# Kernel optimization log

Hardware: AMD Instinct MI355X
Metric: run time of the kernel (lower is better)

The kernel has to match this reference:

```python
import jax, jax.numpy as jnp
import numpy as np

IMG = 224                      # hardcoded image_size in apply_mask
K = int(0.25 * IMG * IMG)      # 12544 pixels masked per sample


def setup_inputs() -> dict:
    key = jax.random.key(0)
    k1, k2 = jax.random.split(key)
    B = 256
    data = jax.random.normal(k1, (B, IMG, IMG, 3), dtype=jnp.float32)
    # |gradients| flattened over (H, W, C) -> length IMG*IMG*3, nonnegative
    line_grad = jax.random.uniform(k2, (B, IMG * IMG * 3), dtype=jnp.float32)
    return {"data": data, "line_grad": line_grad}


def _mask_one(d, g):
    # d: [IMG, IMG, 3], g: [IMG*IMG*3]
    _, idx = jax.lax.top_k(g, K)              # flat indices into (H,W,C)
    reduced = jnp.mod(idx, IMG * IMG)         # fold channel offset -> spatial
    rows = reduced // IMG
    cols = reduced % IMG
    # scatter zeros across all 3 channels at the selected pixels
    return d.at[rows, cols].set(0.0)


def reference(data, line_grad):
    # vectorized_map over the batch -> vmap
    return jax.vmap(_mask_one)(data, line_grad)
```

## Files before the change

kernel.cpp:

```cpp
#include <hip/hip_runtime.h>

#define IMG    224
#define NPIX   (IMG * IMG)
#define NELEM  (NPIX * 3)
#define KSEL   12544
#define NBINS  4096
#define MAXCAND 2048
#define NMASKW (NPIX / 32)
#define NVEC   (NELEM / 4)
#define BLOCK  1024
#define NWAVE  (BLOCK / 64)

typedef float f4 __attribute__((ext_vector_type(4)));

__global__ __launch_bounds__(BLOCK) void masked_model_kernel(
    const float* __restrict__ data,
    const float* __restrict__ grad,
    float* __restrict__ out)
{
    const int b    = blockIdx.x;
    const int tid  = threadIdx.x;
    const int lane = tid & 63;
    const int wid  = tid >> 6;

    const float* g = grad + (size_t)b * NELEM;
    const float* d = data + (size_t)b * NELEM;
    float*       o = out  + (size_t)b * NELEM;

    __shared__ unsigned int hist[NBINS];
    __shared__ unsigned int mask[NMASKW];
    __shared__ unsigned int candkey[MAXCAND];
    __shared__ unsigned int candidx[MAXCAND];
    __shared__ unsigned int wtot[NWAVE];
    __shared__ unsigned int candcnt;
    __shared__ int sB1;
    __shared__ unsigned int sR;

    for (int i = tid; i < NBINS; i += BLOCK) hist[i] = 0u;
    for (int i = tid; i < NMASKW; i += BLOCK) mask[i] = 0u;
    if (tid == 0) candcnt = 0u;
    __syncthreads();

    const f4* g4 = (const f4*)g;

    {
        int i = tid;
        for (; i + 3 * BLOCK < NVEC; i += 4 * BLOCK) {
            f4 v0 = g4[i];
            f4 v1 = g4[i + BLOCK];
            f4 v2 = g4[i + 2 * BLOCK];
            f4 v3 = g4[i + 3 * BLOCK];
            #pragma unroll
            for (int c = 0; c < 4; ++c) atomicAdd(&hist[min((int)(v0[c] * 4096.0f), NBINS - 1)], 1u);
            #pragma unroll
            for (int c = 0; c < 4; ++c) atomicAdd(&hist[min((int)(v1[c] * 4096.0f), NBINS - 1)], 1u);
            #pragma unroll
            for (int c = 0; c < 4; ++c) atomicAdd(&hist[min((int)(v2[c] * 4096.0f), NBINS - 1)], 1u);
            #pragma unroll
            for (int c = 0; c < 4; ++c) atomicAdd(&hist[min((int)(v3[c] * 4096.0f), NBINS - 1)], 1u);
        }
        for (; i < NVEC; i += BLOCK) {
            f4 v = g4[i];
            #pragma unroll
            for (int c = 0; c < 4; ++c) atomicAdd(&hist[min((int)(v[c] * 4096.0f), NBINS - 1)], 1u);
        }
    }
    __syncthreads();

    {
        unsigned int s = hist[4 * tid] + hist[4 * tid + 1]
                       + hist[4 * tid + 2] + hist[4 * tid + 3];

        unsigned int v = s;
        #pragma unroll
        for (int off = 1; off < 64; off <<= 1) {
            unsigned int u = __shfl_down(v, off);
            if (lane + off < 64) v += u;
        }
        if (lane == 0) wtot[wid] = v;
        __syncthreads();

        unsigned int woff = 0;
        for (int w = wid + 1; w < NWAVE; ++w) woff += wtot[w];

        unsigned int a  = v + woff;
        unsigned int nx = a - s;

        if (a >= KSEL && nx < KSEL) {
            unsigned int cum = nx;
            for (int i = 3; i >= 0; --i) {
                unsigned int h = hist[4 * tid + i];
                cum += h;
                if (cum >= KSEL) {
                    sB1 = 4 * tid + i;
                    sR  = KSEL - (cum - h);
                    break;
                }
            }
        }
    }
    __syncthreads();

    {
        const int B1 = sB1;
        auto classify = [&](float val, int idx) {
            int bin = min((int)(val * 4096.0f), NBINS - 1);
            if (bin > B1) {
                int p = idx % NPIX;
                atomicOr(&mask[p >> 5], 1u << (p & 31));
            } else if (bin == B1) {
                unsigned int c2 = atomicAdd(&candcnt, 1u);
                if (c2 < MAXCAND) {
                    candkey[c2] = __float_as_uint(val);
                    candidx[c2] = (unsigned int)idx;
                }
            }
        };
        int i = tid;
        for (; i + 3 * BLOCK < NVEC; i += 4 * BLOCK) {
            f4 v0 = g4[i];
            f4 v1 = g4[i + BLOCK];
            f4 v2 = g4[i + 2 * BLOCK];
            f4 v3 = g4[i + 3 * BLOCK];
            #pragma unroll
            for (int c = 0; c < 4; ++c) classify(v0[c], 4 * i + c);
            #pragma unroll
            for (int c = 0; c < 4; ++c) classify(v1[c], 4 * (i + BLOCK) + c);
            #pragma unroll
            for (int c = 0; c < 4; ++c) classify(v2[c], 4 * (i + 2 * BLOCK) + c);
            #pragma unroll
            for (int c = 0; c < 4; ++c) classify(v3[c], 4 * (i + 3 * BLOCK) + c);
        }
        for (; i < NVEC; i += BLOCK) {
            f4 v = g4[i];
            #pragma unroll
            for (int c = 0; c < 4; ++c) classify(v[c], 4 * i + c);
        }
    }
    __syncthreads();

    {
        unsigned int n = candcnt < MAXCAND ? candcnt : MAXCAND;
        unsigned int r = sR;
        for (unsigned int j = tid; j < n; j += BLOCK) {
            unsigned int kj = candkey[j];
            unsigned int ij = candidx[j];
            unsigned int rank = 0;
            for (unsigned int i = 0; i < n; ++i) {
                unsigned int ki = candkey[i];
                rank += (ki > kj) || (ki == kj && candidx[i] < ij);
            }
            if (rank < r) {
                int p = (int)(ij % NPIX);
                atomicOr(&mask[p >> 5], 1u << (p & 31));
            }
        }
    }
    __syncthreads();

    {
        const f4* d4 = (const f4*)d;
        f4*       o4 = (f4*)o;
        auto apply = [&](f4 v, int i) -> f4 {
            int e = 4 * i;
            int p0 = e / 3, p1 = (e + 1) / 3, p2 = (e + 2) / 3, p3 = (e + 3) / 3;
            if ((mask[p0 >> 5] >> (p0 & 31)) & 1u) v.x = 0.0f;
            if ((mask[p1 >> 5] >> (p1 & 31)) & 1u) v.y = 0.0f;
            if ((mask[p2 >> 5] >> (p2 & 31)) & 1u) v.z = 0.0f;
            if ((mask[p3 >> 5] >> (p3 & 31)) & 1u) v.w = 0.0f;
            return v;
        };
        int i = tid;
        for (; i + 3 * BLOCK < NVEC; i += 4 * BLOCK) {
            f4 v0 = __builtin_nontemporal_load(&d4[i]);
            f4 v1 = __builtin_nontemporal_load(&d4[i + BLOCK]);
            f4 v2 = __builtin_nontemporal_load(&d4[i + 2 * BLOCK]);
            f4 v3 = __builtin_nontemporal_load(&d4[i + 3 * BLOCK]);
            __builtin_nontemporal_store(apply(v0, i),             &o4[i]);
            __builtin_nontemporal_store(apply(v1, i + BLOCK),     &o4[i + BLOCK]);
            __builtin_nontemporal_store(apply(v2, i + 2 * BLOCK), &o4[i + 2 * BLOCK]);
            __builtin_nontemporal_store(apply(v3, i + 3 * BLOCK), &o4[i + 3 * BLOCK]);
        }
        for (; i < NVEC; i += BLOCK) {
            f4 v = d4[i];
            o4[i] = apply(v, i);
        }
    }
}

extern "C" void kernel_launch(void* const* d_in, const int* in_sizes, int n_in,
                              void* d_out, int out_size, void* d_ws, size_t ws_size,
                              hipStream_t stream) {
    const float* data = (const float*)d_in[0];
    const float* grad = (const float*)d_in[1];
    float* out = (float*)d_out;

    const int B = in_sizes[0] / NELEM;
    masked_model_kernel<<<B, BLOCK, 0, stream>>>(data, grad, out);
}
```

Baseline: 373.7 us.

## Split masking into four kernels with two blocks per sample and fused output pass

Replaces the single fused per-sample kernel with a pipeline: a histogram kernel using two blocks per sample that merge into a global histogram, a threshold kernel, an output kernel that reads the three channel gradients per pixel and masks data directly, and a fix-up kernel that ranks boundary-bin candidates and zeroes their pixels in the output. The aim is more blocks in flight (512 instead of 256) and dropping the separate classify pass and shared bitmask. In exchange it adds launch overhead, a workspace memset, global atomics for candidates, and re-reads of the gradient. The old kernel stays as a fallback when the workspace is too small, and MAXCAND is halved.

After: 404.1 us. 8.1% more time.

```diff
diff --git a/kernel.cpp b/kernel.cpp
--- a/kernel.cpp
+++ b/kernel.cpp
@@ -5,13 +5,200 @@
 #define NELEM  (NPIX * 3)
 #define KSEL   12544
 #define NBINS  4096
-#define MAXCAND 2048
-#define NMASKW (NPIX / 32)
-#define NVEC   (NELEM / 4)
+#define MAXCAND 1024
 #define BLOCK  1024
 #define NWAVE  (BLOCK / 64)
+#define SPLIT  2
+#define NPIX4  (NPIX / 4)
+#define GVEC   (NELEM / 4)
+#define HGVEC  (GVEC / SPLIT)
+#define PGRP   (NPIX4 / SPLIT)
 
 typedef float f4 __attribute__((ext_vector_type(4)));
+
+__device__ __forceinline__ int binof(float x) {
+    return min((int)(x * 4096.0f), NBINS - 1);
+}
+
+__global__ __launch_bounds__(BLOCK) void k1_hist(
+    const float* __restrict__ grad, unsigned int* __restrict__ hist)
+{
+    const int smp  = blockIdx.x / SPLIT;
+    const int half = blockIdx.x % SPLIT;
+    const int tid  = threadIdx.x;
+
+    __shared__ unsigned int lh[NBINS];
+    for (int i = tid; i < NBINS; i += BLOCK) lh[i] = 0u;
+    __syncthreads();
+
+    const f4* g4 = (const f4*)(grad + (size_t)smp * NELEM) + (size_t)half * HGVEC;
+
+    int i = tid;
+    for (; i + 3 * BLOCK < HGVEC; i += 4 * BLOCK) {
+        f4 v0 = g4[i];
+        f4 v1 = g4[i + BLOCK];
+        f4 v2 = g4[i + 2 * BLOCK];
+        f4 v3 = g4[i + 3 * BLOCK];
+        #pragma unroll
+        for (int c = 0; c < 4; ++c) atomicAdd(&lh[binof(v0[c])], 1u);
+        #pragma unroll
+        for (int c = 0; c < 4; ++c) atomicAdd(&lh[binof(v1[c])], 1u);
+        #pragma unroll
+        for (int c = 0; c < 4; ++c) atomicAdd(&lh[binof(v2[c])], 1u);
+        #pragma unroll
+        for (int c = 0; c < 4; ++c) atomicAdd(&lh[binof(v3[c])], 1u);
+    }
+    for (; i < HGVEC; i += BLOCK) {
+        f4 v = g4[i];
+        #pragma unroll
+        for (int c = 0; c < 4; ++c) atomicAdd(&lh[binof(v[c])], 1u);
+    }
+    __syncthreads();
+
+    unsigned int* h = hist + (size_t)smp * NBINS;
+    for (int i2 = tid; i2 < NBINS; i2 += BLOCK) atomicAdd(&h[i2], lh[i2]);
+}
+
+__global__ __launch_bounds__(BLOCK) void k2_thresh(
+    const unsigned int* __restrict__ hist,
+    int* __restrict__ B1a, unsigned int* __restrict__ Ra)
+{
+    const int smp  = blockIdx.x;
+    const int tid  = threadIdx.x;
+    const int lane = tid & 63;
+    const int wid  = tid >> 6;
+
+    __shared__ unsigned int wtot[NWAVE];
+
+    uint4 h = ((const uint4*)(hist + (size_t)smp * NBINS))[tid];
+    unsigned int s = h.x + h.y + h.z + h.w;
+
+    unsigned int v = s;
+    #pragma unroll
+    for (int off = 1; off < 64; off <<= 1) {
+        unsigned int u = __shfl_down(v, off);
+        if (lane + off < 64) v += u;
+    }
+    if (lane == 0) wtot[wid] = v;
+    __syncthreads();
+
+    unsigned int woff = 0;
+    for (int w = wid + 1; w < NWAVE; ++w) woff += wtot[w];
+
+    unsigned int a  = v + woff;
+    unsigned int nx = a - s;
+
+    if (a >= KSEL && nx < KSEL) {
+        unsigned int hh[4] = {h.x, h.y, h.z, h.w};
+        unsigned int cum = nx;
+        for (int i = 3; i >= 0; --i) {
+            cum += hh[i];
+            if (cum >= KSEL) {
+                B1a[smp] = 4 * tid + i;
+                Ra[smp]  = KSEL - (cum - hh[i]);
+                break;
+            }
+        }
+    }
+}
+
+__global__ __launch_bounds__(BLOCK) void k3_out(
+    const float* __restrict__ data, const float* __restrict__ grad,
+    float* __restrict__ out,
+    const int* __restrict__ B1a,
+    unsigned int* __restrict__ candcnt,
+    unsigned int* __restrict__ candkey, unsigned int* __restrict__ candidx)
+{
+    const int smp  = blockIdx.x / SPLIT;
+    const int half = blockIdx.x % SPLIT;
+    const int tid  = threadIdx.x;
+    const int B1   = B1a[smp];
+
+    const f4* g4 = (const f4*)(grad + (size_t)smp * NELEM);
+    const f4* d4 = (const f4*)(data + (size_t)smp * NELEM);
+    f4*       o4 = (f4*)(out + (size_t)smp * NELEM);
+
+    unsigned int* ck = candkey + (size_t)smp * MAXCAND;
+    unsigned int* ci = candidx + (size_t)smp * MAXCAND;
+
+    auto push = [&](float val, unsigned int idx) {
+        unsigned int c2 = atomicAdd(&candcnt[smp], 1u);
+        if (c2 < MAXCAND) {
+            ck[c2] = __float_as_uint(val);
+            ci[c2] = idx;
+        }
+    };
+
+    for (int q = tid; q < PGRP; q += BLOCK) {
+        const int G = half * PGRP + q;
+        f4 pa = g4[G];
+        f4 pb = g4[G + NPIX4];
+        f4 pc = g4[G + 2 * NPIX4];
+        f4 x0 = __builtin_nontemporal_load(&d4[3 * G]);
+        f4 x1 = __builtin_nontemporal_load(&d4[3 * G + 1]);
+        f4 x2 = __builtin_nontemporal_load(&d4[3 * G + 2]);
+
+        bool m[4];
+        #pragma unroll
+        for (int j = 0; j < 4; ++j) {
+            int ba = binof(pa[j]);
+            int bb = binof(pb[j]);
+            int bc = binof(pc[j]);
+            m[j] = (ba > B1) || (bb > B1) || (bc > B1);
+            unsigned int p = (unsigned int)(4 * G + j);
+            if (ba == B1) push(pa[j], p);
+            if (bb == B1) push(pb[j], p + NPIX);
+            if (bc == B1) push(pc[j], p + 2 * NPIX);
+        }
+
+        if (m[0]) { x0.x = 0.0f; x0.y = 0.0f; x0.z = 0.0f; }
+        if (m[1]) { x0.w = 0.0f; x1.x = 0.0f; x1.y = 0.0f; }
+        if (m[2]) { x1.z = 0.0f; x1.w = 0.0f; x2.x = 0.0f; }
+        if (m[3]) { x2.y = 0.0f; x2.z = 0.0f; x2.w = 0.0f; }
+
+        __builtin_nontemporal_store(x0, &o4[3 * G]);
+        __builtin_nontemporal_store(x1, &o4[3 * G + 1]);
+        __builtin_nontemporal_store(x2, &o4[3 * G + 2]);
+    }
+}
+
+__global__ __launch_bounds__(256) void k4_fix(
+    float* __restrict__ out,
+    const unsigned int* __restrict__ candcnt,
+    const unsigned int* __restrict__ candkey,
+    const unsigned int* __restrict__ candidx,
+    const unsigned int* __restrict__ Ra)
+{
+    const int smp = blockIdx.x;
+    const int t   = threadIdx.x;
+
+    __shared__ unsigned int sk[MAXCAND];
+    __shared__ unsigned int si[MAXCAND];
+
+    unsigned int n = candcnt[smp];
+    if (n > MAXCAND) n = MAXCAND;
+    unsigned int r = Ra[smp];
+
+    const unsigned int* ck = candkey + (size_t)smp * MAXCAND;
+    const unsigned int* ci = candidx + (size_t)smp * MAXCAND;
+    for (unsigned int j = t; j < n; j += 256) { sk[j] = ck[j]; si[j] = ci[j]; }
+    __syncthreads();
+
+    for (unsigned int j = t; j < n; j += 256) {
+        unsigned int kj = sk[j];
+        unsigned int ij = si[j];
+        unsigned int rank = 0;
+        for (unsigned int i = 0; i < n; ++i) {
+            unsigned int ki = sk[i];
+            rank += (ki > kj) || (ki == kj && si[i] < ij);
+        }
+        if (rank < r) {
+            unsigned int p = ij % NPIX;
+            float* op = out + (size_t)smp * NELEM + 3u * p;
+            op[0] = 0.0f; op[1] = 0.0f; op[2] = 0.0f;
+        }
+    }
+}
 
 __global__ __launch_bounds__(BLOCK) void masked_model_kernel(
     const float* __restrict__ data,
@@ -28,7 +215,7 @@
     float*       o = out  + (size_t)b * NELEM;
 
     __shared__ unsigned int hist[NBINS];
-    __shared__ unsigned int mask[NMASKW];
+    __shared__ unsigned int mask[NPIX / 32];
     __shared__ unsigned int candkey[MAXCAND];
     __shared__ unsigned int candidx[MAXCAND];
     __shared__ unsigned int wtot[NWAVE];
@@ -37,40 +224,21 @@
     __shared__ unsigned int sR;
 
     for (int i = tid; i < NBINS; i += BLOCK) hist[i] = 0u;
-    for (int i = tid; i < NMASKW; i += BLOCK) mask[i] = 0u;
+    for (int i = tid; i < NPIX / 32; i += BLOCK) mask[i] = 0u;
     if (tid == 0) candcnt = 0u;
     __syncthreads();
 
     const f4* g4 = (const f4*)g;
-
-    {
-        int i = tid;
-        for (; i + 3 * BLOCK < NVEC; i += 4 * BLOCK) {
-            f4 v0 = g4[i];
-            f4 v1 = g4[i + BLOCK];
-            f4 v2 = g4[i + 2 * BLOCK];
-            f4 v3 = g4[i + 3 * BLOCK];
-            #pragma unroll
-            for (int c = 0; c < 4; ++c) atomicAdd(&hist[min((int)(v0[c] * 4096.0f), NBINS - 1)], 1u);
-            #pragma unroll
-            for (int c = 0; c < 4; ++c) atomicAdd(&hist[min((int)(v1[c] * 4096.0f), NBINS - 1)], 1u);
-            #pragma unroll
-            for (int c = 0; c < 4; ++c) atomicAdd(&hist[min((int)(v2[c] * 4096.0f), NBINS - 1)], 1u);
-            #pragma unroll
-            for (int c = 0; c < 4; ++c) atomicAdd(&hist[min((int)(v3[c] * 4096.0f), NBINS - 1)], 1u);
-        }
-        for (; i < NVEC; i += BLOCK) {
-            f4 v = g4[i];
-            #pragma unroll
-            for (int c = 0; c < 4; ++c) atomicAdd(&hist[min((int)(v[c] * 4096.0f), NBINS - 1)], 1u);
-        }
+    for (int i = tid; i < GVEC; i += BLOCK) {
+        f4 v = g4[i];
+        #pragma unroll
+        for (int c = 0; c < 4; ++c) atomicAdd(&hist[binof(v[c])], 1u);
     }
     __syncthreads();
 
     {
         unsigned int s = hist[4 * tid] + hist[4 * tid + 1]
                        + hist[4 * tid + 2] + hist[4 * tid + 3];
-
         unsigned int v = s;
         #pragma unroll
         for (int off = 1; off < 64; off <<= 1) {
@@ -79,23 +247,16 @@
         }
         if (lane == 0) wtot[wid] = v;
         __syncthreads();
-
         unsigned int woff = 0;
         for (int w = wid + 1; w < NWAVE; ++w) woff += wtot[w];
-
         unsigned int a  = v + woff;
         unsigned int nx = a - s;
-
         if (a >= KSEL && nx < KSEL) {
             unsigned int cum = nx;
             for (int i = 3; i >= 0; --i) {
                 unsigned int h = hist[4 * tid + i];
                 cum += h;
-                if (cum >= KSEL) {
-                    sB1 = 4 * tid + i;
-                    sR  = KSEL - (cum - h);
-                    break;
-                }
+                if (cum >= KSEL) { sB1 = 4 * tid + i; sR = KSEL - (cum - h); break; }
             }
         }
     }
@@ -103,38 +264,23 @@
 
     {
         const int B1 = sB1;
-        auto classify = [&](float val, int idx) {
-            int bin = min((int)(val * 4096.0f), NBINS - 1);
-            if (bin > B1) {
-                int p = idx % NPIX;
-                atomicOr(&mask[p >> 5], 1u << (p & 31));
-            } else if (bin == B1) {
-                unsigned int c2 = atomicAdd(&candcnt, 1u);
-                if (c2 < MAXCAND) {
-                    candkey[c2] = __float_as_uint(val);
-                    candidx[c2] = (unsigned int)idx;
-                }
-            }
-        };
-        int i = tid;
-        for (; i + 3 * BLOCK < NVEC; i += 4 * BLOCK) {
-            f4 v0 = g4[i];
-            f4 v1 = g4[i + BLOCK];
-            f4 v2 = g4[i + 2 * BLOCK];
-            f4 v3 = g4[i + 3 * BLOCK];
-            #pragma unroll
-            for (int c = 0; c < 4; ++c) classify(v0[c], 4 * i + c);
-            #pragma unroll
-            for (int c = 0; c < 4; ++c) classify(v1[c], 4 * (i + BLOCK) + c);
-            #pragma unroll
-            for (int c = 0; c < 4; ++c) classify(v2[c], 4 * (i + 2 * BLOCK) + c);
-            #pragma unroll
-            for (int c = 0; c < 4; ++c) classify(v3[c], 4 * (i + 3 * BLOCK) + c);
-        }
-        for (; i < NVEC; i += BLOCK) {
+        for (int i = tid; i < GVEC; i += BLOCK) {
             f4 v = g4[i];
             #pragma unroll
-            for (int c = 0; c < 4; ++c) classify(v[c], 4 * i + c);
+            for (int c = 0; c < 4; ++c) {
+                int bin = binof(v[c]);
+                int idx = 4 * i + c;
+                if (bin > B1) {
+                    int p = idx % NPIX;
+                    atomicOr(&mask[p >> 5], 1u << (p & 31));
+                } else if (bin == B1) {
+                    unsigned int c2 = atomicAdd(&candcnt, 1u);
+                    if (c2 < MAXCAND) {
+                        candkey[c2] = __float_as_uint(v[c]);
+                        candidx[c2] = (unsigned int)idx;
+                    }
+                }
+            }
         }
     }
     __syncthreads();
@@ -161,29 +307,15 @@
     {
         const f4* d4 = (const f4*)d;
         f4*       o4 = (f4*)o;
-        auto apply = [&](f4 v, int i) -> f4 {
+        for (int i = tid; i < GVEC; i += BLOCK) {
+            f4 v = d4[i];
             int e = 4 * i;
             int p0 = e / 3, p1 = (e + 1) / 3, p2 = (e + 2) / 3, p3 = (e + 3) / 3;
             if ((mask[p0 >> 5] >> (p0 & 31)) & 1u) v.x = 0.0f;
             if ((mask[p1 >> 5] >> (p1 & 31)) & 1u) v.y = 0.0f;
             if ((mask[p2 >> 5] >> (p2 & 31)) & 1u) v.z = 0.0f;
             if ((mask[p3 >> 5] >> (p3 & 31)) & 1u) v.w = 0.0f;
-            return v;
-        };
-        int i = tid;
-        for (; i + 3 * BLOCK < NVEC; i += 4 * BLOCK) {
-            f4 v0 = __builtin_nontemporal_load(&d4[i]);
-            f4 v1 = __builtin_nontemporal_load(&d4[i + BLOCK]);
-            f4 v2 = __builtin_nontemporal_load(&d4[i + 2 * BLOCK]);
-            f4 v3 = __builtin_nontemporal_load(&d4[i + 3 * BLOCK]);
-            __builtin_nontemporal_store(apply(v0, i),             &o4[i]);
-            __builtin_nontemporal_store(apply(v1, i + BLOCK),     &o4[i + BLOCK]);
-            __builtin_nontemporal_store(apply(v2, i + 2 * BLOCK), &o4[i + 2 * BLOCK]);
-            __builtin_nontemporal_store(apply(v3, i + 3 * BLOCK), &o4[i + 3 * BLOCK]);
-        }
-        for (; i < NVEC; i += BLOCK) {
-            f4 v = d4[i];
-            o4[i] = apply(v, i);
+            o4[i] = v;
         }
     }
 }
@@ -196,5 +328,29 @@
     float* out = (float*)d_out;
 
     const int B = in_sizes[0] / NELEM;
-    masked_model_kernel<<<B, BLOCK, 0, stream>>>(data, grad, out);
-}
+
+    const size_t histB  = (size_t)B * NBINS * 4;
+    const size_t cntB   = (size_t)B * 4;
+    const size_t candB  = (size_t)B * MAXCAND * 4;
+    const size_t needed = histB + 3 * cntB + 2 * candB;
+
+    if (ws_size < needed) {
+        masked_model_kernel<<<B, BLOCK, 0, stream>>>(data, grad, out);
+        return;
+    }
+
+    char* ws = (char*)d_ws;
+    unsigned int* hist    = (unsigned int*)(ws);
+    unsigned int* candcnt = (unsigned int*)(ws + histB);
+    int*          B1a     = (int*)         (ws + histB + cntB);
+    unsigned int* Ra      = (unsigned int*)(ws + histB + 2 * cntB);
+    unsigned int* candkey = (unsigned int*)(ws + histB + 3 * cntB);
+    unsigned int* candidx = (unsigned int*)(ws + histB + 3 * cntB + candB);
+
+    hipMemsetAsync(ws, 0, histB + cntB, stream);
+
+    k1_hist  <<<B * SPLIT, BLOCK, 0, stream>>>(grad, hist);
+    k2_thresh<<<B,         BLOCK, 0, stream>>>(hist, B1a, Ra);
+    k3_out   <<<B * SPLIT, BLOCK, 0, stream>>>(data, grad, out, B1a, candcnt, candkey, candidx);
+    k4_fix   <<<B,         256,   0, stream>>>(out, candcnt, candkey, candidx, Ra);
+}
```
